# Optimization experiments

Measured on AMD Instinct MI355X. Metric: run time of the kernel, lower is better.

The kernel has to match this reference:

```python
import jax, jax.numpy as jnp
import numpy as np

KH = KW = 3
SH = SW = 1
PH = PW = 1
EPS = 1e-6


def _unfold(x, kh, kw, sh, sw, ph, pw):
    """Replicates torch.nn.functional.unfold: returns [B, C*kh*kw, L]."""
    x = jnp.pad(x, ((0, 0), (0, 0), (ph, ph), (pw, pw)))
    B, C, H, W = x.shape
    Ho = (H - kh) // sh + 1
    Wo = (W - kw) // sw + 1
    # channel-major, then (kh, kw) ordering, matching F.unfold
    cols = jnp.stack(
        [x[:, :, i:i + (Ho - 1) * sh + 1:sh, j:j + (Wo - 1) * sw + 1:sw]
         for i in range(kh) for j in range(kw)],
        axis=2,
    )  # [B, C, kh*kw, Ho, Wo]
    return cols.reshape(B, C * kh * kw, Ho * Wo), Ho, Wo


def setup_inputs() -> dict:
    key = jax.random.key(0)
    k1, k2, k3 = jax.random.split(key, 3)
    x = jax.random.normal(k1, (4, 32, 32, 32), dtype=jnp.float32)
    positions = jax.random.uniform(k2, (32, 32, 3, 3, 5), dtype=jnp.float32,
                                   minval=-1.0, maxval=1.0)
    values = jax.random.normal(k3, (32, 32, 3, 3, 5), dtype=jnp.float32) * 0.01
    return {"x": x, "positions": positions, "values": values}


def _piecewise_conv(x, positions, values):
    O, C, kh, kw, P = positions.shape
    patches, Ho, Wo = _unfold(x, KH, KW, SH, SW, PH, PW)  # [B, T, L]
    T = C * kh * kw
    B = x.shape[0]
    L = Ho * Wo

    pos = positions.reshape(O, T, P)
    val = values.reshape(O, T, P)
    # forward sorts each (out_ch, input) table by position
    order = jnp.argsort(pos, axis=-1)
    pos = jnp.take_along_axis(pos, order, axis=-1)
    val = jnp.take_along_axis(val, order, axis=-1)

    xv = patches.transpose(0, 2, 1)          # [B, L, T]
    xb = xv[:, None, :, :]                   # [B, 1, L, T]

    # interval index: last j with pos[j] <= x (== count(pos <= x) - 1)
    cnt = jnp.sum(pos[None, :, None, :, :] <= xb[..., None], axis=-1)  # [B,O,L,T]
    idx = jnp.clip(cnt - 1, 0, P - 2)

    def gather(tab, ind):
        # tab: [O, T, P], ind: [B, O, L, T] -> [B, O, L, T]
        ind2 = ind.transpose(1, 3, 0, 2).reshape(O, T, B * L)
        out = jnp.take_along_axis(tab, ind2, axis=-1)
        return out.reshape(O, T, B, L).transpose(2, 0, 3, 1)

    pos_j = gather(pos, idx)
    pos_j1 = gather(pos, idx + 1)
    val_j = gather(val, idx)
    val_j1 = gather(val, idx + 1)

    t = jnp.clip((xb - pos_j) / (pos_j1 - pos_j + EPS), 0.0, 1.0)
    interp = val_j + t * (val_j1 - val_j)
    res = jnp.where(pos_j == pos_j1, val_j, interp)

    first = pos[None, :, None, :, 0]
    last = pos[None, :, None, :, P - 1]
    v0 = val[None, :, None, :, 0]
    vl = val[None, :, None, :, P - 1]
    res = jnp.where(xb <= first, v0, jnp.where(xb >= last, vl, res))

    out = res.sum(axis=-1)                   # [B, O, L]
    return out.reshape(B, O, Ho, Wo)


def reference(x, positions, values):
    return _piecewise_conv(x, positions, values)
```

## Files before the change

### kernel.cpp

```cpp
#include <hip/hip_runtime.h>

#define B_  4
#define O_  32
#define C_  32
#define H_  32
#define W_  32
#define P_  5
#define T_  288
#define EPSF 1e-6f

#define NCH 4
#define CG  (C_ / NCH)


__global__ __launch_bounds__(256) void zero_out(float* __restrict__ out, int n)
{
    int i = blockIdx.x * 256 + threadIdx.x;
    if (i < n) out[i] = 0.f;
}

__global__ __launch_bounds__(256) void prep_tables(
    const float* __restrict__ pos, const float* __restrict__ val,
    float* __restrict__ tab)
{
    int id = blockIdx.x * 256 + threadIdx.x;
    if (id >= O_ * T_) return;

    const float* pp = pos + id * P_;
    const float* vv = val + id * P_;
    float p0 = pp[0], p1 = pp[1], p2 = pp[2], p3 = pp[3], p4 = pp[4];
    float v0 = vv[0], v1 = vv[1], v2 = vv[2], v3 = vv[3], v4 = vv[4];

#define CSWAP(a, b, va, vb)                         \
    {                                               \
        float _pa = fminf(a, b), _pb = fmaxf(a, b); \
        bool _sw = (a > b);                         \
        float _va = _sw ? vb : va;                  \
        float _vb = _sw ? va : vb;                  \
        a = _pa; b = _pb; va = _va; vb = _vb;       \
    }
    CSWAP(p0, p1, v0, v1);
    CSWAP(p3, p4, v3, v4);
    CSWAP(p2, p4, v2, v4);
    CSWAP(p2, p3, v2, v3);
    CSWAP(p1, p4, v1, v4);
    CSWAP(p0, p3, v0, v3);
    CSWAP(p0, p2, v0, v2);
    CSWAP(p1, p3, v1, v3);
    CSWAP(p1, p2, v1, v2);
#undef CSWAP

    float inv0 = 1.0f / (p1 - p0 + EPSF);
    float inv1 = 1.0f / (p2 - p1 + EPSF);
    float inv2 = 1.0f / (p3 - p2 + EPSF);
    float inv3 = 1.0f / (p4 - p3 + EPSF);

    float* e = tab + id * 16;
    e[0]  = inv0;        e[1]  = inv1;        e[2]  = inv2;        e[3]  = inv3;
    e[4]  = -p0 * inv0;  e[5]  = -p1 * inv1;  e[6]  = -p2 * inv2;  e[7]  = -p3 * inv3;
    e[8]  = v1 - v0;     e[9]  = v2 - v1;     e[10] = v3 - v2;     e[11] = v4 - v3;
    e[12] = v0;          e[13] = 0.f;         e[14] = 0.f;         e[15] = 0.f;
}

#define XROW 34
#define XSTR 35
#define XS_PER_CH (XROW * XSTR)

__global__ __launch_bounds__(256, 4) void pw_conv(
    const float* __restrict__ x, const float* __restrict__ tab,
    float* __restrict__ out)
{
    __shared__ float xs[NCH * XS_PER_CH];

    const int cg = blockIdx.x;
    const int o  = blockIdx.y;
    const int b  = blockIdx.z;
    const int tid = threadIdx.x;
    const int c0 = cg * NCH;

    const float* xb = x + (b * C_ + c0) * (H_ * W_);
    for (int idx = tid; idx < NCH * XROW * XROW; idx += 256) {
        int ch  = idx / (XROW * XROW);
        int rem = idx - ch * (XROW * XROW);
        int r   = rem / XROW;
        int col = rem - r * XROW;
        int gr = r - 1, gc = col - 1;
        float v = 0.f;
        if ((unsigned)gr < (unsigned)H_ && (unsigned)gc < (unsigned)W_)
            v = xb[ch * (H_ * W_) + gr * W_ + gc];
        xs[ch * XS_PER_CH + r * XSTR + col] = v;
    }
    __syncthreads();

    const int r  = tid >> 3;
    const int c4 = (tid & 7) * 4;
    const float* tb = tab + (o * T_ + c0 * 9) * 16;

    float acc0 = 0.f, acc1 = 0.f, acc2 = 0.f, acc3 = 0.f;

    for (int ch = 0; ch < NCH; ++ch) {
        float xr[3][6];
#pragma unroll
        for (int i = 0; i < 3; ++i)
#pragma unroll
            for (int j = 0; j < 6; ++j)
                xr[i][j] = xs[ch * XS_PER_CH + (r + i) * XSTR + c4 + j];

        const float* ec = tb + ch * 9 * 16;
#pragma unroll
        for (int ij = 0; ij < 9; ++ij) {
            const int i = ij / 3, j = ij % 3;
            const float* e = ec + ij * 16;
            float i0 = e[0], i1 = e[1], i2 = e[2], i3 = e[3];
            float f0 = e[4], f1 = e[5], f2 = e[6], f3 = e[7];
            float d0 = e[8], d1 = e[9], d2 = e[10], d3 = e[11];
            float v0 = e[12];

#define EVAL(ACC, XV)                                                      \
            {                                                              \
                float _xv = (XV);                                          \
                ACC += v0;                                                 \
                float _t;                                                  \
                _t = fmaf(_xv, i0, f0);                                    \
                _t = fminf(fmaxf(_t, 0.f), 1.f); ACC = fmaf(_t, d0, ACC);  \
                _t = fmaf(_xv, i1, f1);                                    \
                _t = fminf(fmaxf(_t, 0.f), 1.f); ACC = fmaf(_t, d1, ACC);  \
                _t = fmaf(_xv, i2, f2);                                    \
                _t = fminf(fmaxf(_t, 0.f), 1.f); ACC = fmaf(_t, d2, ACC);  \
                _t = fmaf(_xv, i3, f3);                                    \
                _t = fminf(fmaxf(_t, 0.f), 1.f); ACC = fmaf(_t, d3, ACC);  \
            }
            EVAL(acc0, xr[i][j + 0]);
            EVAL(acc1, xr[i][j + 1]);
            EVAL(acc2, xr[i][j + 2]);
            EVAL(acc3, xr[i][j + 3]);
#undef EVAL
        }
    }

    float* op = out + (b * O_ + o) * (H_ * W_) + r * W_ + c4;
    __hip_atomic_fetch_add(op + 0, acc0, __ATOMIC_RELAXED, __HIP_MEMORY_SCOPE_AGENT);
    __hip_atomic_fetch_add(op + 1, acc1, __ATOMIC_RELAXED, __HIP_MEMORY_SCOPE_AGENT);
    __hip_atomic_fetch_add(op + 2, acc2, __ATOMIC_RELAXED, __HIP_MEMORY_SCOPE_AGENT);
    __hip_atomic_fetch_add(op + 3, acc3, __ATOMIC_RELAXED, __HIP_MEMORY_SCOPE_AGENT);
}

extern "C" void kernel_launch(void* const* d_in, const int* in_sizes, int n_in,
                              void* d_out, int out_size, void* d_ws, size_t ws_size,
                              hipStream_t stream)
{
    const float* x   = (const float*)d_in[0];
    const float* pos = (const float*)d_in[1];
    const float* val = (const float*)d_in[2];
    float* tab = (float*)d_ws;

    zero_out<<<(out_size + 255) / 256, 256, 0, stream>>>((float*)d_out, out_size);

    prep_tables<<<(O_ * T_ + 255) / 256, 256, 0, stream>>>(pos, val, tab);

    dim3 grid(CG, O_, B_);
    pw_conv<<<grid, 256, 0, stream>>>(x, tab, (float*)d_out);
}
```

Measured before the change: 90.95 us.

## Compute 2x4 output tile per thread with 128-thread blocks and vector table loads

Each thread now computes a 2-row by 4-column output tile, reusing a 4x6 window of shared-memory inputs, so blocks shrink to 128 threads. The channel group per block is halved so there are twice as many blocks, and table entries are loaded as float4. The aim is to amortise table loads and shared-memory reads over more outputs. In exchange, register pressure rises and the doubled block count doubles the number of atomic adds to the output.

```diff
diff --git a/kernel.cpp b/kernel.cpp
--- a/kernel.cpp
+++ b/kernel.cpp
@@ -9,7 +9,7 @@
 #define T_  288
 #define EPSF 1e-6f
 
-#define NCH 4
+#define NCH 2
 #define CG  (C_ / NCH)
 
 
@@ -66,7 +66,7 @@
 #define XSTR 35
 #define XS_PER_CH (XROW * XSTR)
 
-__global__ __launch_bounds__(256, 4) void pw_conv(
+__global__ __launch_bounds__(128, 6) void pw_conv(
     const float* __restrict__ x, const float* __restrict__ tab,
     float* __restrict__ out)
 {
@@ -79,7 +79,7 @@
     const int c0 = cg * NCH;
 
     const float* xb = x + (b * C_ + c0) * (H_ * W_);
-    for (int idx = tid; idx < NCH * XROW * XROW; idx += 256) {
+    for (int idx = tid; idx < NCH * XROW * XROW; idx += 128) {
         int ch  = idx / (XROW * XROW);
         int rem = idx - ch * (XROW * XROW);
         int r   = rem / XROW;
@@ -92,57 +92,57 @@
     }
     __syncthreads();
 
-    const int r  = tid >> 3;
+    const int r0 = (tid >> 3) * 2;
     const int c4 = (tid & 7) * 4;
     const float* tb = tab + (o * T_ + c0 * 9) * 16;
 
-    float acc0 = 0.f, acc1 = 0.f, acc2 = 0.f, acc3 = 0.f;
+    float acc[2][4] = {{0.f, 0.f, 0.f, 0.f}, {0.f, 0.f, 0.f, 0.f}};
 
+#pragma unroll
     for (int ch = 0; ch < NCH; ++ch) {
-        float xr[3][6];
+        float xw[4][6];
 #pragma unroll
-        for (int i = 0; i < 3; ++i)
+        for (int i = 0; i < 4; ++i)
 #pragma unroll
             for (int j = 0; j < 6; ++j)
-                xr[i][j] = xs[ch * XS_PER_CH + (r + i) * XSTR + c4 + j];
+                xw[i][j] = xs[ch * XS_PER_CH + (r0 + i) * XSTR + c4 + j];
 
-        const float* ec = tb + ch * 9 * 16;
+        const float4* e4 = (const float4*)(tb + ch * 9 * 16);
 #pragma unroll
         for (int ij = 0; ij < 9; ++ij) {
             const int i = ij / 3, j = ij % 3;
-            const float* e = ec + ij * 16;
-            float i0 = e[0], i1 = e[1], i2 = e[2], i3 = e[3];
-            float f0 = e[4], f1 = e[5], f2 = e[6], f3 = e[7];
-            float d0 = e[8], d1 = e[9], d2 = e[10], d3 = e[11];
-            float v0 = e[12];
+            const float4 qi = e4[ij * 4 + 0];
+            const float4 qf = e4[ij * 4 + 1];
+            const float4 qd = e4[ij * 4 + 2];
+            const float4 qv = e4[ij * 4 + 3];
 
-#define EVAL(ACC, XV)                                                      \
-            {                                                              \
-                float _xv = (XV);                                          \
-                ACC += v0;                                                 \
-                float _t;                                                  \
-                _t = fmaf(_xv, i0, f0);                                    \
-                _t = fminf(fmaxf(_t, 0.f), 1.f); ACC = fmaf(_t, d0, ACC);  \
-                _t = fmaf(_xv, i1, f1);                                    \
-                _t = fminf(fmaxf(_t, 0.f), 1.f); ACC = fmaf(_t, d1, ACC);  \
-                _t = fmaf(_xv, i2, f2);                                    \
-                _t = fminf(fmaxf(_t, 0.f), 1.f); ACC = fmaf(_t, d2, ACC);  \
-                _t = fmaf(_xv, i3, f3);                                    \
-                _t = fminf(fmaxf(_t, 0.f), 1.f); ACC = fmaf(_t, d3, ACC);  \
-            }
-            EVAL(acc0, xr[i][j + 0]);
-            EVAL(acc1, xr[i][j + 1]);
-            EVAL(acc2, xr[i][j + 2]);
-            EVAL(acc3, xr[i][j + 3]);
-#undef EVAL
+#pragma unroll
+            for (int dr = 0; dr < 2; ++dr)
+#pragma unroll
+                for (int dc = 0; dc < 4; ++dc) {
+                    float xv = xw[dr + i][dc + j];
+                    float a  = acc[dr][dc] + qv.x;
+                    float t;
+                    t = fmaf(xv, qi.x, qf.x);
+                    t = fminf(fmaxf(t, 0.f), 1.f); a = fmaf(t, qd.x, a);
+                    t = fmaf(xv, qi.y, qf.y);
+                    t = fminf(fmaxf(t, 0.f), 1.f); a = fmaf(t, qd.y, a);
+                    t = fmaf(xv, qi.z, qf.z);
+                    t = fminf(fmaxf(t, 0.f), 1.f); a = fmaf(t, qd.z, a);
+                    t = fmaf(xv, qi.w, qf.w);
+                    t = fminf(fmaxf(t, 0.f), 1.f); a = fmaf(t, qd.w, a);
+                    acc[dr][dc] = a;
+                }
         }
     }
 
-    float* op = out + (b * O_ + o) * (H_ * W_) + r * W_ + c4;
-    __hip_atomic_fetch_add(op + 0, acc0, __ATOMIC_RELAXED, __HIP_MEMORY_SCOPE_AGENT);
-    __hip_atomic_fetch_add(op + 1, acc1, __ATOMIC_RELAXED, __HIP_MEMORY_SCOPE_AGENT);
-    __hip_atomic_fetch_add(op + 2, acc2, __ATOMIC_RELAXED, __HIP_MEMORY_SCOPE_AGENT);
-    __hip_atomic_fetch_add(op + 3, acc3, __ATOMIC_RELAXED, __HIP_MEMORY_SCOPE_AGENT);
+    float* op = out + (b * O_ + o) * (H_ * W_);
+#pragma unroll
+    for (int dr = 0; dr < 2; ++dr)
+#pragma unroll
+        for (int dc = 0; dc < 4; ++dc)
+            __hip_atomic_fetch_add(op + (r0 + dr) * W_ + c4 + dc, acc[dr][dc],
+                                   __ATOMIC_RELAXED, __HIP_MEMORY_SCOPE_AGENT);
 }
 
 extern "C" void kernel_launch(void* const* d_in, const int* in_sizes, int n_in,
@@ -159,5 +159,5 @@
     prep_tables<<<(O_ * T_ + 255) / 256, 256, 0, stream>>>(pos, val, tab);
 
     dim3 grid(CG, O_, B_);
-    pw_conv<<<grid, 256, 0, stream>>>(x, tab, (float*)d_out);
+    pw_conv<<<grid, 128, 0, stream>>>(x, tab, (float*)d_out);
 }
```

Result: slower. 95.69 us (+5.2%).
